# Kernel optimization log

Measured on AMD Instinct MI355X. Metric: run time of the kernel, lower is better.

Reference implementation:

```python
import jax, jax.numpy as jnp
import numpy as np

N = 1024
BATCH = 16384


def setup_inputs() -> dict:
    key = jax.random.key(0)
    k1, k2 = jax.random.split(key)
    log_alpha = jax.random.normal(k1, (BATCH, N), dtype=jnp.float32)
    W = jax.random.normal(k2, (N, N), dtype=jnp.float32)  # unnormalized_transition_matrix
    return {"log_alpha": log_alpha, "W": W}


def reference(log_alpha, W):
    # log_softmax over dim=0 (columns sum to 1 in prob space)
    logT = jax.nn.log_softmax(W, axis=0)  # [N, N]
    # log-domain matmul: out[b, i] = logsumexp_k( logT[i, k] + log_alpha[b, k] )
    # Stable exp-shift trick avoids materializing the [B, N, N] broadcast tensor:
    mA = jnp.max(logT, axis=1, keepdims=True)        # [N, 1] row max of logT
    mB = jnp.max(log_alpha, axis=1, keepdims=True)   # [B, 1] row max of log_alpha
    expA = jnp.exp(logT - mA)                        # [N, N]
    expB = jnp.exp(log_alpha - mB)                   # [B, N]
    s = jnp.einsum('bk,ik->bi', expB, expA)          # [B, N]
    return jnp.log(s) + mB + mA.T                    # [B, N]
```

## Files before the change

### kernel.cpp

```cpp
#include <hip/hip_runtime.h>
#include <hip/hip_bf16.h>
#include <stdint.h>

#define MB_ 16384
#define NN_ 1024
#define KK_ 1024

typedef __bf16 bhalf;
typedef __bf16 bhalf8 __attribute__((ext_vector_type(8)));
typedef __bf16 bhalf4 __attribute__((ext_vector_type(4)));
typedef float f32x4 __attribute__((ext_vector_type(4)));

typedef const __attribute__((address_space(1))) void* gas_ptr;
typedef __attribute__((address_space(3))) void* las_ptr;

__device__ __forceinline__ void gload_lds16(const void* g, void* l) {
  __builtin_amdgcn_global_load_lds((gas_ptr)g, (las_ptr)l, 16, 0, 0);
}

__global__ void k_colpart(const float* __restrict__ W,
                          float* __restrict__ pM, float* __restrict__ pS) {
  int col = blockIdx.x * 256 + threadIdx.x;
  int rc  = blockIdx.y;
  const float* p = W + (size_t)rc * 32 * NN_ + col;
  float v[32];
#pragma unroll
  for (int i = 0; i < 32; ++i) v[i] = p[(size_t)i * NN_];
  float m = v[0];
#pragma unroll
  for (int i = 1; i < 32; ++i) m = fmaxf(m, v[i]);
  float s = 0.f;
#pragma unroll
  for (int i = 0; i < 32; ++i) s += __expf(v[i] - m);
  pM[rc * NN_ + col] = m;
  pS[rc * NN_ + col] = s;
}

__global__ void k_colfin(const float* __restrict__ pM, const float* __restrict__ pS,
                         float* __restrict__ colLSE) {
  int col = blockIdx.x * 256 + threadIdx.x;
  float m = -1e30f;
#pragma unroll
  for (int i = 0; i < 32; ++i) m = fmaxf(m, pM[i * NN_ + col]);
  float s = 0.f;
#pragma unroll
  for (int i = 0; i < 32; ++i) s += pS[i * NN_ + col] * __expf(pM[i * NN_ + col] - m);
  colLSE[col] = m + __logf(s);
}

__global__ void k_expA(const float* __restrict__ W, const float* __restrict__ colLSE,
                       bhalf* __restrict__ eA) {
  int i = blockIdx.x;
  int l = threadIdx.x;
  const float4* row = (const float4*)(W + (size_t)i * NN_);
  const float4* cls = (const float4*)colLSE;
#pragma unroll
  for (int t = 0; t < 4; ++t) {
    float4 wv = row[t * 64 + l];
    float4 cv = cls[t * 64 + l];
    bhalf4 o;
    o[0] = (bhalf)__expf(wv.x - cv.x);
    o[1] = (bhalf)__expf(wv.y - cv.y);
    o[2] = (bhalf)__expf(wv.z - cv.z);
    o[3] = (bhalf)__expf(wv.w - cv.w);
    *(bhalf4*)(eA + (size_t)i * NN_ + t * 256 + l * 4) = o;
  }
}


#define VMW(N)  asm volatile("s_waitcnt vmcnt(" #N ")" ::: "memory")
#define LGKM0   asm volatile("s_waitcnt lgkmcnt(0)" ::: "memory")
#define HINT8   asm volatile("s_waitcnt lgkmcnt(8)" ::: "memory")
#define SBAR    __builtin_amdgcn_s_barrier()
#define SCB0    __builtin_amdgcn_sched_barrier(0)
#define NOPS    ((void)0)

#define STB(BUF, H, TOFF) do {                                                \
    const bhalf* g_ = pgB + (H) * 131072 + (TOFF) * 64;                       \
    unsigned char* d_ = lds + 65536 + (BUF) * 32768 + (H) * 16384 + tid * 16; \
    gload_lds16(g_, d_); gload_lds16(g_ + 65536, d_ + 8192); } while (0)

#define LOADA(TOFF) do {                                                      \
    _Pragma("unroll")                                                         \
    for (int r_ = 0; r_ < 8; ++r_) va[r_] = pLA4[r_ * 8192 + (TOFF) * 16];    \
  } while (0)

#define CVTA(BUF) do {                                                        \
    unsigned char* d_ = dA_base + (BUF) * 32768;                              \
    _Pragma("unroll")                                                         \
    for (int r_ = 0; r_ < 8; ++r_) {                                          \
      float4 u_ = va[r_];                                                     \
      bhalf4 o_;                                                              \
      o_[0] = (bhalf)__expf(u_.x); o_[1] = (bhalf)__expf(u_.y);               \
      o_[2] = (bhalf)__expf(u_.z); o_[3] = (bhalf)__expf(u_.w);               \
      *(bhalf4*)(d_ + (r_ & 3) * 4096 + (r_ >> 2) * 16384) = o_;              \
    } } while (0)

#define DS_AF(BUF, Q)                                                         \
  af[0][0] = *(const bhalf8*)(pA0 + (BUF) * 32768 + (Q) * 4096);              \
  af[0][1] = *(const bhalf8*)(pA1 + (BUF) * 32768 + (Q) * 4096);              \
  af[1][0] = *(const bhalf8*)(pA0 + (BUF) * 32768 + (Q) * 4096 + 2048);       \
  af[1][1] = *(const bhalf8*)(pA1 + (BUF) * 32768 + (Q) * 4096 + 2048);

#define DS_BQ(BUF)                                                            \
  _Pragma("unroll")                                                           \
  for (int n_ = 0; n_ < 4; ++n_) {                                            \
    bq[n_][0] = *(const bhalf8*)(pB0 + (BUF) * 32768 + n_ * 2048);            \
    bq[n_][1] = *(const bhalf8*)(pB1 + (BUF) * 32768 + n_ * 2048);            \
  }

#define MFMA8(Q)                                                              \
  __builtin_amdgcn_s_setprio(1);                                              \
  _Pragma("unroll")                                                           \
  for (int m_ = 0; m_ < 2; ++m_)                                              \
    _Pragma("unroll")                                                         \
    for (int n_ = 0; n_ < 4; ++n_)                                            \
      _Pragma("unroll")                                                       \
      for (int kk_ = 0; kk_ < 2; ++kk_)                                       \
        acc[2 * (Q) + m_][n_] = __builtin_amdgcn_mfma_f32_16x16x32_bf16(      \
            af[m_][kk_], bq[n_][kk_], acc[2 * (Q) + m_][n_], 0, 0, 0);        \
  __builtin_amdgcn_s_setprio(0);

#define HEAD  SCB0; SBAR; LGKM0; SCB0

#define KTILE(BUF, LT, BT, VMN)                                               \
  {                                                                           \
    bhalf8 bq[4][2];                                                          \
    bhalf8 af[2][2];                                                          \
    DS_AF(BUF, 0) DS_BQ(BUF)                                                  \
    if ((LT) >= 0) LOADA(LT);                                                 \
    HINT8;                                                                    \
    HEAD; MFMA8(0) SBAR;                                                      \
    DS_AF(BUF, 1)                                                             \
    if ((BT) >= 0) STB(BUF, 0, BT);                                           \
    HEAD; MFMA8(1) SBAR;                                                      \
    DS_AF(BUF, 2)                                                             \
    if ((BT) >= 0) STB(BUF, 1, BT);                                           \
    HEAD; MFMA8(2) SBAR;                                                      \
    DS_AF(BUF, 3)                                                             \
    HEAD; MFMA8(3)                                                            \
    if ((VMN) == 4) VMW(4); else if ((VMN) == 0) VMW(0);                      \
    if ((LT) >= 0) { CVTA((BUF) ^ 1); LGKM0; }                                \
    SCB0; SBAR;                                                               \
  }

__global__ __launch_bounds__(512, 2) void k_gemm(const float* __restrict__ LA,
                                                 const bhalf* __restrict__ Bt,
                                                 float* __restrict__ out) {
  __shared__ __align__(16) unsigned char lds[131072];

  const int nwg = gridDim.x;
  const int wg  = blockIdx.x;
  const int swz = (wg & 7) * (nwg >> 3) + (wg >> 3);
  const int bm = swz >> 2;
  const int bn = swz & 3;

  const int tid = threadIdx.x;
  const int l = tid & 63;
  const int w = tid >> 6;
  const int wr = w >> 2;
  const int wc = w & 3;

  const int r8  = tid >> 3;
  const int kel = (((tid & 7) ^ (r8 & 7)) << 3);
  const bhalf* pgB = Bt + (size_t)(bn * 256 + r8) * KK_ + kel;

  const float4* pLA4 = (const float4*)(LA + (size_t)(bm * 256 + (tid >> 4)) * KK_) + (tid & 15);
  unsigned char* dA_base = lds + (tid >> 4) * 128 +
                           ((((tid & 15) >> 1) ^ ((tid >> 4) & 7)) << 4) + ((tid & 1) << 3);

  const int kx  = 16 * (l >> 4);
  const int x16 = (l & 7) << 4;
  const int kx0 = kx ^ x16;
  const int kx1 = (64 + kx) ^ x16;
  const unsigned char* pA0 = lds + wr * 16384 + (l & 15) * 128 + kx0;
  const unsigned char* pA1 = lds + wr * 16384 + (l & 15) * 128 + kx1;
  const unsigned char* pB0 = lds + 65536 + (wc >> 1) * 16384 + ((wc & 1) * 64 + (l & 15)) * 128 + kx0;
  const unsigned char* pB1 = lds + 65536 + (wc >> 1) * 16384 + ((wc & 1) * 64 + (l & 15)) * 128 + kx1;

  f32x4 zero = {0.f, 0.f, 0.f, 0.f};
  f32x4 acc[8][4];
#pragma unroll
  for (int m = 0; m < 8; ++m)
#pragma unroll
    for (int n = 0; n < 4; ++n) acc[m][n] = zero;

  float4 va[8];

  LOADA(0);
  STB(0, 0, 0); STB(0, 1, 0);
  STB(1, 0, 1); STB(1, 1, 1);
  VMW(8);
  CVTA(0);
  VMW(4);
  LGKM0;
  SBAR;

  for (int p = 0; p < 7; ++p) {
    KTILE(0, 1, 2, 4)
    KTILE(1, 2, 3, 4)
    pLA4 += 32;
    pgB  += 128;
  }
  KTILE(0, 1, -1, 0)
  KTILE(1, -1, -1, -1)

  const int c0 = bn * 256 + wc * 64 + (l & 15);
  const int r0 = bm * 256 + wr * 128 + (l >> 4) * 4;
#pragma unroll
  for (int mf = 0; mf < 8; ++mf) {
#pragma unroll
    for (int r = 0; r < 4; ++r) {
      const int row = r0 + mf * 16 + r;
      float* o = out + (size_t)row * NN_ + c0;
#pragma unroll
      for (int nf = 0; nf < 4; ++nf)
        __builtin_nontemporal_store(__logf(acc[mf][nf][r]), o + nf * 16);
    }
  }
}

extern "C" void kernel_launch(void* const* d_in, const int* in_sizes, int n_in,
                              void* d_out, int out_size, void* d_ws, size_t ws_size,
                              hipStream_t stream) {
  const float* log_alpha = (const float*)d_in[0];
  const float* W         = (const float*)d_in[1];
  float* out = (float*)d_out;

  uintptr_t ws = (uintptr_t)d_ws;
  bhalf* eA     = (bhalf*)(ws);
  float* colLSE = (float*)(ws + 2097152);
  float* pM     = (float*)(ws + 2101248);
  float* pS     = (float*)(ws + 2232320);

  k_colpart<<<dim3(4, 32), 256, 0, stream>>>(W, pM, pS);
  k_colfin<<<4, 256, 0, stream>>>(pM, pS, colLSE);
  k_expA<<<NN_, 64, 0, stream>>>(W, colLSE, eA);
  k_gemm<<<(MB_ / 256) * (NN_ / 256), 512, 0, stream>>>(log_alpha, eA, out);
}
```

Before: 67.93 us.

## Shrink GEMM K-tile to 32 with 64KB LDS and simpler single-barrier pipeline

Restructures the fused exp+GEMM kernel to use K-tiles of 32 instead of 64. This halves LDS use to 64KB and replaces the four sub-phase barrier schedule with one MFMA block per tile, alongside a new swizzle layout for A and B. It also replaces the nontemporal output stores with plain stores. The goal is less LDS pressure and fewer barriers per tile, at the cost of twice as many loop iterations and waits per K.

```diff
diff --git a/kernel.cpp b/kernel.cpp
--- a/kernel.cpp
+++ b/kernel.cpp
@@ -75,79 +75,59 @@
 #define SCB0    __builtin_amdgcn_sched_barrier(0)
 #define NOPS    ((void)0)
 
-#define STB(BUF, H, TOFF) do {                                                \
-    const bhalf* g_ = pgB + (H) * 131072 + (TOFF) * 64;                       \
-    unsigned char* d_ = lds + 65536 + (BUF) * 32768 + (H) * 16384 + tid * 16; \
-    gload_lds16(g_, d_); gload_lds16(g_ + 65536, d_ + 8192); } while (0)
-
-#define LOADA(TOFF) do {                                                      \
-    _Pragma("unroll")                                                         \
-    for (int r_ = 0; r_ < 8; ++r_) va[r_] = pLA4[r_ * 8192 + (TOFF) * 16];    \
-  } while (0)
-
-#define CVTA(BUF) do {                                                        \
-    unsigned char* d_ = dA_base + (BUF) * 32768;                              \
-    _Pragma("unroll")                                                         \
-    for (int r_ = 0; r_ < 8; ++r_) {                                          \
-      float4 u_ = va[r_];                                                     \
-      bhalf4 o_;                                                              \
-      o_[0] = (bhalf)__expf(u_.x); o_[1] = (bhalf)__expf(u_.y);               \
-      o_[2] = (bhalf)__expf(u_.z); o_[3] = (bhalf)__expf(u_.w);               \
-      *(bhalf4*)(d_ + (r_ & 3) * 4096 + (r_ >> 2) * 16384) = o_;              \
-    } } while (0)
-
-#define DS_AF(BUF, Q)                                                         \
-  af[0][0] = *(const bhalf8*)(pA0 + (BUF) * 32768 + (Q) * 4096);              \
-  af[0][1] = *(const bhalf8*)(pA1 + (BUF) * 32768 + (Q) * 4096);              \
-  af[1][0] = *(const bhalf8*)(pA0 + (BUF) * 32768 + (Q) * 4096 + 2048);       \
-  af[1][1] = *(const bhalf8*)(pA1 + (BUF) * 32768 + (Q) * 4096 + 2048);
-
-#define DS_BQ(BUF)                                                            \
-  _Pragma("unroll")                                                           \
-  for (int n_ = 0; n_ < 4; ++n_) {                                            \
-    bq[n_][0] = *(const bhalf8*)(pB0 + (BUF) * 32768 + n_ * 2048);            \
-    bq[n_][1] = *(const bhalf8*)(pB1 + (BUF) * 32768 + n_ * 2048);            \
-  }
-
-#define MFMA8(Q)                                                              \
-  __builtin_amdgcn_s_setprio(1);                                              \
-  _Pragma("unroll")                                                           \
-  for (int m_ = 0; m_ < 2; ++m_)                                              \
+#define STB(OB, T) do {                                                       \
+    const bhalf* g_ = pgB + (T) * 32;                                         \
+    unsigned char* d_ = lds + 32768 + (OB) * 16384 + tid * 16;                \
+    gload_lds16(g_, d_); gload_lds16(g_ + 131072, d_ + 8192); } while (0)
+
+#define LOADA(T) do {                                                         \
+    _Pragma("unroll")                                                         \
+    for (int j_ = 0; j_ < 4; ++j_) va[j_] = pLA4[(T) * 8 + j_]; } while (0)
+
+#define CVTA(OB) do {                                                         \
+    unsigned char* d_ = lds + (OB) * 16384 + dA_off;                          \
+    bhalf8 o0, o1;                                                            \
+    o0[0] = (bhalf)__expf(va[0].x); o0[1] = (bhalf)__expf(va[0].y);           \
+    o0[2] = (bhalf)__expf(va[0].z); o0[3] = (bhalf)__expf(va[0].w);           \
+    o0[4] = (bhalf)__expf(va[1].x); o0[5] = (bhalf)__expf(va[1].y);           \
+    o0[6] = (bhalf)__expf(va[1].z); o0[7] = (bhalf)__expf(va[1].w);           \
+    o1[0] = (bhalf)__expf(va[2].x); o1[1] = (bhalf)__expf(va[2].y);           \
+    o1[2] = (bhalf)__expf(va[2].z); o1[3] = (bhalf)__expf(va[2].w);           \
+    o1[4] = (bhalf)__expf(va[3].x); o1[5] = (bhalf)__expf(va[3].y);           \
+    o1[6] = (bhalf)__expf(va[3].z); o1[7] = (bhalf)__expf(va[3].w);           \
+    *(bhalf8*)(d_ + aw0) = o0; *(bhalf8*)(d_ + aw1) = o1; } while (0)
+
+#define KTILE(BUF, LT, BT, WA, WB, CV)                                        \
+  {                                                                           \
+    bhalf8 af[8]; bhalf8 bq[4];                                               \
+    if ((LT) >= 0) LOADA(LT);                                                 \
+    if ((BT) >= 0) STB((BUF) ^ 1, BT);                                        \
+    _Pragma("unroll")                                                         \
+    for (int m_ = 0; m_ < 8; ++m_)                                            \
+      af[m_] = *(const bhalf8*)(pA + (BUF) * 16384 + m_ * 1024);              \
     _Pragma("unroll")                                                         \
     for (int n_ = 0; n_ < 4; ++n_)                                            \
+      bq[n_] = *(const bhalf8*)(pB + (BUF) * 16384 + n_ * 1024);              \
+    HINT8;                                                                    \
+    SCB0; SBAR; LGKM0; SCB0;                                                  \
+    __builtin_amdgcn_s_setprio(1);                                            \
+    _Pragma("unroll")                                                         \
+    for (int m_ = 0; m_ < 8; ++m_)                                            \
       _Pragma("unroll")                                                       \
-      for (int kk_ = 0; kk_ < 2; ++kk_)                                       \
-        acc[2 * (Q) + m_][n_] = __builtin_amdgcn_mfma_f32_16x16x32_bf16(      \
-            af[m_][kk_], bq[n_][kk_], acc[2 * (Q) + m_][n_], 0, 0, 0);        \
-  __builtin_amdgcn_s_setprio(0);
-
-#define HEAD  SCB0; SBAR; LGKM0; SCB0
-
-#define KTILE(BUF, LT, BT, VMN)                                               \
-  {                                                                           \
-    bhalf8 bq[4][2];                                                          \
-    bhalf8 af[2][2];                                                          \
-    DS_AF(BUF, 0) DS_BQ(BUF)                                                  \
-    if ((LT) >= 0) LOADA(LT);                                                 \
-    HINT8;                                                                    \
-    HEAD; MFMA8(0) SBAR;                                                      \
-    DS_AF(BUF, 1)                                                             \
-    if ((BT) >= 0) STB(BUF, 0, BT);                                           \
-    HEAD; MFMA8(1) SBAR;                                                      \
-    DS_AF(BUF, 2)                                                             \
-    if ((BT) >= 0) STB(BUF, 1, BT);                                           \
-    HEAD; MFMA8(2) SBAR;                                                      \
-    DS_AF(BUF, 3)                                                             \
-    HEAD; MFMA8(3)                                                            \
-    if ((VMN) == 4) VMW(4); else if ((VMN) == 0) VMW(0);                      \
-    if ((LT) >= 0) { CVTA((BUF) ^ 1); LGKM0; }                                \
+      for (int n_ = 0; n_ < 4; ++n_)                                          \
+        acc[m_][n_] = __builtin_amdgcn_mfma_f32_16x16x32_bf16(                \
+            af[m_], bq[n_], acc[m_][n_], 0, 0, 0);                            \
+    __builtin_amdgcn_s_setprio(0);                                            \
+    WA;                                                                       \
+    if (CV) { CVTA((BUF) ^ 1); LGKM0; }                                       \
+    WB;                                                                       \
     SCB0; SBAR;                                                               \
   }
 
 __global__ __launch_bounds__(512, 2) void k_gemm(const float* __restrict__ LA,
                                                  const bhalf* __restrict__ Bt,
                                                  float* __restrict__ out) {
-  __shared__ __align__(16) unsigned char lds[131072];
+  __shared__ __align__(16) unsigned char lds[65536];
 
   const int nwg = gridDim.x;
   const int wg  = blockIdx.x;
@@ -161,22 +141,20 @@
   const int wr = w >> 2;
   const int wc = w & 3;
 
-  const int r8  = tid >> 3;
-  const int kel = (((tid & 7) ^ (r8 & 7)) << 3);
-  const bhalf* pgB = Bt + (size_t)(bn * 256 + r8) * KK_ + kel;
-
-  const float4* pLA4 = (const float4*)(LA + (size_t)(bm * 256 + (tid >> 4)) * KK_) + (tid & 15);
-  unsigned char* dA_base = lds + (tid >> 4) * 128 +
-                           ((((tid & 15) >> 1) ^ ((tid >> 4) & 7)) << 4) + ((tid & 1) << 3);
-
-  const int kx  = 16 * (l >> 4);
-  const int x16 = (l & 7) << 4;
-  const int kx0 = kx ^ x16;
-  const int kx1 = (64 + kx) ^ x16;
-  const unsigned char* pA0 = lds + wr * 16384 + (l & 15) * 128 + kx0;
-  const unsigned char* pA1 = lds + wr * 16384 + (l & 15) * 128 + kx1;
-  const unsigned char* pB0 = lds + 65536 + (wc >> 1) * 16384 + ((wc & 1) * 64 + (l & 15)) * 128 + kx0;
-  const unsigned char* pB1 = lds + 65536 + (wc >> 1) * 16384 + ((wc & 1) * 64 + (l & 15)) * 128 + kx1;
+  const bhalf* pgB = Bt + (size_t)(bn * 256 + (tid >> 2)) * KK_ +
+                     (((tid & 3) ^ ((tid >> 3) & 3)) << 3);
+
+  const int ar = tid >> 1;
+  const int h  = tid & 1;
+  const float4* pLA4 = (const float4*)(LA + (size_t)(bm * 256 + ar) * KK_) + h * 4;
+  const int dA_off = ar * 64;
+  const int sA = (ar >> 1) & 3;
+  const int aw0 = ((2 * h) ^ sA) << 4;
+  const int aw1 = ((2 * h + 1) ^ sA) << 4;
+
+  const int cs16 = (((l >> 4) ^ (((l & 15) >> 1) & 3)) << 4);
+  const unsigned char* pA = lds + (wr * 128 + (l & 15)) * 64 + cs16;
+  const unsigned char* pB = lds + 32768 + (wc * 64 + (l & 15)) * 64 + cs16;
 
   f32x4 zero = {0.f, 0.f, 0.f, 0.f};
   f32x4 acc[8][4];
@@ -185,25 +163,27 @@
 #pragma unroll
     for (int n = 0; n < 4; ++n) acc[m][n] = zero;
 
-  float4 va[8];
+  float4 va[4];
 
   LOADA(0);
-  STB(0, 0, 0); STB(0, 1, 0);
-  STB(1, 0, 1); STB(1, 1, 1);
-  VMW(8);
+  STB(0, 0);
+  VMW(2);
   CVTA(0);
-  VMW(4);
+  LOADA(1);
+  STB(1, 1);
+  VMW(6);
   LGKM0;
   SBAR;
 
-  for (int p = 0; p < 7; ++p) {
-    KTILE(0, 1, 2, 4)
-    KTILE(1, 2, 3, 4)
-    pLA4 += 32;
-    pgB  += 128;
-  }
-  KTILE(0, 1, -1, 0)
-  KTILE(1, -1, -1, -1)
+  KTILE(0, -1, -1, VMW(2), VMW(0), 1)
+
+  for (int p = 0; p < 15; ++p) {
+    KTILE(1, 2, 2, VMW(2), VMW(0), 1)
+    KTILE(0, 3, 3, VMW(2), VMW(0), 1)
+    pLA4 += 16;
+    pgB  += 64;
+  }
+  KTILE(1, -1, -1, NOPS, NOPS, 0)
 
   const int c0 = bn * 256 + wc * 64 + (l & 15);
   const int r0 = bm * 256 + wr * 128 + (l >> 4) * 4;
@@ -215,7 +195,7 @@
       float* o = out + (size_t)row * NN_ + c0;
 #pragma unroll
       for (int nf = 0; nf < 4; ++nf)
-        __builtin_nontemporal_store(__logf(acc[mf][nf][r]), o + nf * 16);
+        o[nf * 16] = __logf(acc[mf][nf][r]);
     }
   }
 }
```

Result: faster. 65.24 us (-4.0%).
